# Performance work log

Hardware: AMD Instinct MI355X
Metric: run time of the kernel (lower is better)

The kernel has to match this reference:

```python
import jax, jax.numpy as jnp
import numpy as np

IN_FEATURES = 4096
OUT_FEATURES = 11008


def setup_inputs() -> dict:
    key = jax.random.key(0)
    k1, k2, k3, k4 = jax.random.split(key, 4)
    x = jax.random.normal(k1, (2, 2048, IN_FEATURES), dtype=jnp.float32)
    # two signed int4 values packed per byte: low nibble = even k, high nibble = odd k
    w_packed = jax.random.randint(k2, (OUT_FEATURES, IN_FEATURES // 2), 0, 256, dtype=jnp.int32)
    # rowwise dequant scales (positive, roughly max|w|/7 scale)
    w_scales = jax.random.uniform(k3, (OUT_FEATURES,), dtype=jnp.float32, minval=0.001, maxval=0.02)
    bias = jax.random.normal(k4, (OUT_FEATURES,), dtype=jnp.float32)
    return {"x": x, "w_packed": w_packed, "w_scales": w_scales, "bias": bias}


def _dequantize(w_packed, w_scales):
    # unpack two int4 nibbles per byte
    low = w_packed & 0xF            # [O, K//2]
    high = (w_packed >> 4) & 0xF    # [O, K//2]
    q = jnp.stack([low, high], axis=-1).reshape(w_packed.shape[0], -1)  # [O, K]
    q = jnp.where(q >= 8, q - 16, q)  # sign-extend int4 to [-8, 7]
    return q.astype(w_scales.dtype) * w_scales[:, None]  # [O, K]


def reference(x, w_packed, w_scales, bias):
    w = _dequantize(w_packed, w_scales)               # [O, K] fp32
    y = jnp.einsum('bsk,ok->bso', x, w)               # GEMM
    return y + bias
```

## Files before the change

### kernel.cpp

```cpp
#include <hip/hip_runtime.h>
#include <hip/hip_bf16.h>
#include <stdint.h>

#define M_DIM 4096
#define K_DIM 4096
#define N_DIM 11008
#define KP    2048

#define BK2   64
#define NKT   (K_DIM/BK2)
#define NTM2  (M_DIM/256)
#define NTN2  (N_DIM/256)
#define NBLK2 (NTM2*NTN2)
#define HT_BYTES 8192

#define BM 128
#define BN 128
#define BK 64
#define NTM (M_DIM/BM)
#define NTN (N_DIM/BN)
#define NBLK (NTM*NTN)

typedef __attribute__((ext_vector_type(8)))  short bf16x8;
typedef __attribute__((ext_vector_type(4)))  float f32x4;
typedef __attribute__((ext_vector_type(4)))  int   i32x4;
typedef __attribute__((ext_vector_type(16))) int   i32x16;
typedef __attribute__((ext_vector_type(16))) char  c8x16;
typedef __attribute__((ext_vector_type(8)))  unsigned short u16x8;

typedef const void __attribute__((address_space(1)))* gas_ptr;
typedef void __attribute__((address_space(3)))* las_ptr;

__device__ __forceinline__ void async_copy16(void* lds, const void* g) {
  __builtin_amdgcn_global_load_lds((gas_ptr)g, (las_ptr)lds, 16, 0, 0);
}

__device__ __forceinline__ unsigned short f2bf_rne(float f) {
  uint32_t u = __builtin_bit_cast(uint32_t, f);
  u += 0x7FFFu + ((u >> 16) & 1u);
  return (unsigned short)(u >> 16);
}
__device__ __forceinline__ unsigned short i2bf(int v) {
  float f = (float)v;
  return (unsigned short)(__builtin_bit_cast(uint32_t, f) >> 16);
}
__device__ __forceinline__ int sx4(int b, int which) {
  return ((int)((uint32_t)b << (28 - 4 * which))) >> 28;
}


__global__ __launch_bounds__(256) void rowmax_x(const float* __restrict__ x,
                                                float* __restrict__ xs,
                                                float* __restrict__ xr) {
  const int row = blockIdx.x;
  const int tid = threadIdx.x;
  const float4* r4 = (const float4*)(x + (size_t)row * K_DIM);
  float m = 0.f;
  for (int j = tid; j < K_DIM / 4; j += 256) {
    float4 v = r4[j];
    m = fmaxf(m, fmaxf(fmaxf(fabsf(v.x), fabsf(v.y)), fmaxf(fabsf(v.z), fabsf(v.w))));
  }
  for (int off = 32; off >= 1; off >>= 1) m = fmaxf(m, __shfl_down(m, off));
  __shared__ float sm[4];
  if ((tid & 63) == 0) sm[tid >> 6] = m;
  __syncthreads();
  if (tid == 0) {
    m = fmaxf(fmaxf(sm[0], sm[1]), fmaxf(sm[2], sm[3]));
    xs[row] = m * (1.0f / 127.0f);
    xr[row] = (m > 0.f) ? 127.0f / m : 0.f;
  }
}

__global__ __launch_bounds__(256) void quant_x_tiled(const float* __restrict__ x,
                                                     const float* __restrict__ xr,
                                                     char* __restrict__ wsA) {
  const int total = NTM2 * NKT * 2 * 512;
  for (int i = blockIdx.x * blockDim.x + threadIdx.x; i < total;
       i += gridDim.x * blockDim.x) {
    int rc  = i & 511;
    int h   = (i >> 9) & 1;
    int kt  = (i >> 10) & 63;
    int tm  = i >> 16;
    int row = rc >> 2, e = rc & 3;
    int grow = tm * 256 + h * 128 + row;
    const float4* src = (const float4*)(x + (size_t)grow * K_DIM + kt * 64 + e * 16);
    float4 v0 = src[0], v1 = src[1], v2 = src[2], v3 = src[3];
    float vv[16] = { v0.x, v0.y, v0.z, v0.w, v1.x, v1.y, v1.z, v1.w,
                     v2.x, v2.y, v2.z, v2.w, v3.x, v3.y, v3.z, v3.w };
    const float rs = xr[grow];
    c8x16 q;
#pragma unroll
    for (int j = 0; j < 16; ++j) q[j] = (char)__float2int_rn(vv[j] * rs);
    int c = (row >> 5) * 128 + (e >> 1) * 64 + (e & 1) * 32 + (row & 31);
    *(c8x16*)(wsA + (size_t)(i >> 9) * HT_BYTES + c * 16) = q;
  }
}

__global__ __launch_bounds__(256) void deq_w_i8(const int* __restrict__ wp,
                                                char* __restrict__ wsB) {
  const int total = NTN2 * NKT * 2 * 512;
  for (int i = blockIdx.x * blockDim.x + threadIdx.x; i < total;
       i += gridDim.x * blockDim.x) {
    int rc  = i & 511;
    int h   = (i >> 9) & 1;
    int kt  = (i >> 10) & 63;
    int tn  = i >> 16;
    int row = rc >> 2, e = rc & 3;
    const int4* src = (const int4*)(wp + (size_t)(tn * 256 + h * 128 + row) * KP + kt * 32 + e * 8);
    int4 a = src[0], b = src[1];
    c8x16 q;
    q[0]  = (char)sx4(a.x, 0); q[1]  = (char)sx4(a.x, 1);
    q[2]  = (char)sx4(a.y, 0); q[3]  = (char)sx4(a.y, 1);
    q[4]  = (char)sx4(a.z, 0); q[5]  = (char)sx4(a.z, 1);
    q[6]  = (char)sx4(a.w, 0); q[7]  = (char)sx4(a.w, 1);
    q[8]  = (char)sx4(b.x, 0); q[9]  = (char)sx4(b.x, 1);
    q[10] = (char)sx4(b.y, 0); q[11] = (char)sx4(b.y, 1);
    q[12] = (char)sx4(b.z, 0); q[13] = (char)sx4(b.z, 1);
    q[14] = (char)sx4(b.w, 0); q[15] = (char)sx4(b.w, 1);
    int c = (row >> 5) * 128 + (e >> 1) * 64 + (e & 1) * 32 + (row & 31);
    *(c8x16*)(wsB + (size_t)(i >> 9) * HT_BYTES + c * 16) = q;
  }
}

__global__ __launch_bounds__(512, 2)
void qgemm8i(const char* __restrict__ wsA, const char* __restrict__ wsB,
             const float* __restrict__ xs,
             const float* __restrict__ scales, const float* __restrict__ bias,
             float* __restrict__ out) {
  __shared__ __align__(16) char smem[65536];

  const int tid  = threadIdx.x;
  const int lane = tid & 63, wid = tid >> 6;
  const int wr = wid >> 2, wc = wid & 3;
  const int l31 = lane & 31, kg = lane >> 5;

  int bid = blockIdx.x;
  int id  = (bid & 7) * (NBLK2 / 8) + (bid >> 3);
  int tm  = id & (NTM2 - 1), tn = id >> 4;

  const char* gA = wsA + (size_t)tm * (NKT * 2) * HT_BYTES;
  const char* gB = wsB + (size_t)tn * (NKT * 2) * HT_BYTES;

  const char* baseA = smem + wr * HT_BYTES + lane * 16;
  const char* baseB = smem + 16384 + (wc >> 1) * HT_BYTES + lane * 16;

#define STAGE(ldsoff, src) \
    async_copy16(smem + (ldsoff) + wid * 1024, (src) + wid * 1024 + lane * 16)
#define STAGE_A(buf, h, kt) STAGE((buf) * 32768 + (h) * HT_BYTES, gA + ((kt) * 2 + (h)) * HT_BYTES)
#define STAGE_B(buf, h, kt) STAGE((buf) * 32768 + 16384 + (h) * HT_BYTES, gB + ((kt) * 2 + (h)) * HT_BYTES)

  i32x16 acc[4][2] = {};
  i32x4  aS0[2][2], aS1[2][2];
  i32x4  bS0[2], bS1[2];

#define LDA_SET(dst, buf, sel) do { \
    _Pragma("unroll") for (int i = 0; i < 2; ++i) \
    _Pragma("unroll") for (int ks = 0; ks < 2; ++ks) \
      dst[i][ks] = *(const i32x4*)(baseA + (buf) * 32768 + ((sel) * 2 + i) * 2048 + ks * 1024); \
  } while (0)
#define LDB_SET(dst, buf, bn) do { \
    _Pragma("unroll") for (int ks = 0; ks < 2; ++ks) \
      dst[ks] = *(const i32x4*)(baseB + (buf) * 32768 + ((wc & 1) * 2 + (bn)) * 2048 + ks * 1024); \
  } while (0)
#define MMQ(aS, bS, sel, bn) do { \
    _Pragma("unroll") for (int ks = 0; ks < 2; ++ks) \
    _Pragma("unroll") for (int i = 0; i < 2; ++i) \
      acc[(sel) * 2 + i][bn] = __builtin_amdgcn_mfma_i32_32x32x32_i8( \
          aS[i][ks], bS[ks], acc[(sel) * 2 + i][bn], 0, 0, 0); \
  } while (0)

#define PH_BAR __builtin_amdgcn_s_barrier()
#define LGKM0 asm volatile("s_waitcnt lgkmcnt(0)" ::: "memory")
#define VMC1  asm volatile("s_waitcnt vmcnt(1)" ::: "memory")
#define VMC2  asm volatile("s_waitcnt vmcnt(2)" ::: "memory")
#define PRIO1 __builtin_amdgcn_s_setprio(1)
#define PRIO0 __builtin_amdgcn_s_setprio(0)

  STAGE_B(0, 0, 0); STAGE_B(0, 1, 0);
  STAGE_A(0, 0, 0); STAGE_A(0, 1, 0);
  STAGE_B(1, 0, 1); STAGE_B(1, 1, 1);
  VMC2;
  PH_BAR;
  LDA_SET(aS0, 0, 0); LDB_SET(bS0, 0, 0);

  for (int t = 0; t < NKT / 2; ++t) {
    const int k1 = 2 * t + 1;
    const int k2 = (2 * t + 2 < NKT) ? 2 * t + 2 : NKT - 1;
    const int k3 = (2 * t + 3 < NKT) ? 2 * t + 3 : NKT - 1;

    LGKM0; PRIO1; MMQ(aS0, bS0, 0, 0); PRIO0;
    STAGE_A(1, 0, k1);
    LDB_SET(bS1, 0, 1);
    PH_BAR;
    LGKM0; PRIO1; MMQ(aS0, bS1, 0, 1); PRIO0;
    STAGE_A(1, 1, k1);
    LDA_SET(aS1, 0, 1);
    PH_BAR;
    LGKM0; PRIO1; MMQ(aS1, bS1, 1, 1); PRIO0;
    STAGE_B(0, 0, k2);
    VMC1;
    PH_BAR;
    PRIO1; MMQ(aS1, bS0, 1, 0); PRIO0;
    STAGE_B(0, 1, k2);
    LDA_SET(aS0, 1, 0); LDB_SET(bS0, 1, 0);
    PH_BAR;
    LGKM0; PRIO1; MMQ(aS0, bS0, 0, 0); PRIO0;
    STAGE_A(0, 0, k2);
    LDB_SET(bS1, 1, 1);
    PH_BAR;
    LGKM0; PRIO1; MMQ(aS0, bS1, 0, 1); PRIO0;
    STAGE_A(0, 1, k2);
    LDA_SET(aS1, 1, 1);
    PH_BAR;
    LGKM0; PRIO1; MMQ(aS1, bS1, 1, 1); PRIO0;
    STAGE_B(1, 0, k3);
    VMC1;
    PH_BAR;
    PRIO1; MMQ(aS1, bS0, 1, 0); PRIO0;
    STAGE_B(1, 1, k3);
    LDA_SET(aS0, 0, 0); LDB_SET(bS0, 0, 0);
    PH_BAR;
  }

  const int m0 = tm * 256, n0 = tn * 256;
#pragma unroll
  for (int ni = 0; ni < 2; ++ni) {
    const int o = n0 + wc * 64 + ni * 32 + l31;
    const float sw = scales[o];
    const float b = bias[o];
#pragma unroll
    for (int mi = 0; mi < 4; ++mi) {
      const int mrb = m0 + wr * 128 + mi * 32 + kg * 4;
#pragma unroll
      for (int r = 0; r < 16; ++r) {
        const int mr = mrb + (r & 3) + 8 * (r >> 2);
        const float y = (float)acc[mi][ni][r] * xs[mr] * sw + b;
        __builtin_nontemporal_store(y, out + (size_t)mr * N_DIM + o);
      }
    }
  }
#undef STAGE
#undef STAGE_A
#undef STAGE_B
#undef LDA_SET
#undef LDB_SET
#undef MMQ
#undef PH_BAR
#undef LGKM0
#undef VMC1
#undef VMC2
#undef PRIO1
#undef PRIO0
}

__global__ __launch_bounds__(256) void cvt_x_kernel(const float* __restrict__ x,
                                                    unsigned short* __restrict__ xb) {
  const int n4 = M_DIM * K_DIM / 4;
  int i = blockIdx.x * blockDim.x + threadIdx.x;
  const int stride = gridDim.x * blockDim.x;
  for (; i < n4; i += stride) {
    float4 v = ((const float4*)x)[i];
    ushort4 r;
    r.x = f2bf_rne(v.x); r.y = f2bf_rne(v.y);
    r.z = f2bf_rne(v.z); r.w = f2bf_rne(v.w);
    ((ushort4*)xb)[i] = r;
  }
}

template <int MODE>
__global__ __launch_bounds__(256)
void qgemm_kernel(const float* __restrict__ x, const unsigned short* __restrict__ xb,
                  const int* __restrict__ wp,
                  const float* __restrict__ scales, const float* __restrict__ bias,
                  float* __restrict__ out) {
  __shared__ __align__(16) unsigned short As[BM * BK];
  __shared__ __align__(16) unsigned short Bs[BN * BK];
  const int tid  = threadIdx.x;
  const int lane = tid & 63;
  const int wid  = tid >> 6;
  int bid = blockIdx.x;
  int swzb = (bid & 7) * (NBLK / 8) + (bid >> 3);
  const int tm = swzb & (NTM - 1);
  const int tn = swzb >> 5;
  const int m0 = tm * BM, n0 = tn * BN;
  const int wr = wid >> 1, wc = wid & 1;
  const int fr = lane & 15;
  const int fg = lane >> 4;
  f32x4 acc[4][4] = {};

  for (int kt = 0; kt < K_DIM / BK; ++kt) {
    int4   breg[4];
    float4 areg[8];
#pragma unroll
    for (int p = 0; p < 4; ++p) {
      int fl = p * 256 + tid;
      int row = fl >> 3, u = fl & 7;
      breg[p] = *(const int4*)(wp + (size_t)(n0 + row) * KP + kt * (BK / 2) + u * 4);
    }
    if constexpr (MODE == 2) {
#pragma unroll
      for (int p = 0; p < 8; ++p) {
        int fl = p * 256 + tid;
        int row = fl >> 4, u = fl & 15;
        areg[p] = *(const float4*)(x + (size_t)(m0 + row) * K_DIM + kt * BK + u * 4);
      }
    }
    __syncthreads();
    if constexpr (MODE == 1) {
#pragma unroll
      for (int p = 0; p < 4; ++p) {
        int t16 = p * 256 + tid;
        int row = t16 >> 3, u = t16 & 7;
        const unsigned short* g = xb + (size_t)(m0 + row) * K_DIM + kt * BK + u * 8;
        async_copy16((char*)As + (p * 256 + wid * 64) * 16, g);
      }
    } else {
#pragma unroll
      for (int p = 0; p < 8; ++p) {
        int fl = p * 256 + tid;
        int row = fl >> 4, u = fl & 15;
        ushort4 r;
        r.x = f2bf_rne(areg[p].x); r.y = f2bf_rne(areg[p].y);
        r.z = f2bf_rne(areg[p].z); r.w = f2bf_rne(areg[p].w);
        *(ushort4*)((char*)As + row * 128 + u * 8) = r;
      }
    }
#pragma unroll
    for (int p = 0; p < 4; ++p) {
      int fl = p * 256 + tid;
      int row = fl >> 3, u = fl & 7;
      int4 b = breg[p];
      u16x8 r;
      r[0] = i2bf(sx4(b.x, 0)); r[1] = i2bf(sx4(b.x, 1));
      r[2] = i2bf(sx4(b.y, 0)); r[3] = i2bf(sx4(b.y, 1));
      r[4] = i2bf(sx4(b.z, 0)); r[5] = i2bf(sx4(b.z, 1));
      r[6] = i2bf(sx4(b.w, 0)); r[7] = i2bf(sx4(b.w, 1));
      *(u16x8*)((char*)Bs + row * 128 + u * 16) = r;
    }
    __syncthreads();
#pragma unroll
    for (int kk = 0; kk < 2; ++kk) {
      const int kb = kk * 64 + fg * 16;
      bf16x8 af[4], bfv[4];
#pragma unroll
      for (int mi = 0; mi < 4; ++mi) {
        int row = wr * 64 + mi * 16 + fr;
        af[mi] = *(const bf16x8*)((const char*)As + row * 128 + kb);
      }
#pragma unroll
      for (int ni = 0; ni < 4; ++ni) {
        int row = wc * 64 + ni * 16 + fr;
        bfv[ni] = *(const bf16x8*)((const char*)Bs + row * 128 + kb);
      }
#pragma unroll
      for (int mi = 0; mi < 4; ++mi)
#pragma unroll
        for (int ni = 0; ni < 4; ++ni)
          acc[mi][ni] = __builtin_amdgcn_mfma_f32_16x16x32_bf16(af[mi], bfv[ni], acc[mi][ni], 0, 0, 0);
    }
  }
#pragma unroll
  for (int ni = 0; ni < 4; ++ni) {
    const int o = n0 + wc * 64 + ni * 16 + fr;
    const float s = scales[o];
    const float b = bias[o];
#pragma unroll
    for (int mi = 0; mi < 4; ++mi) {
      const int mr = m0 + wr * 64 + mi * 16 + fg * 4;
#pragma unroll
      for (int r = 0; r < 4; ++r)
        out[(size_t)(mr + r) * N_DIM + o] = acc[mi][ni][r] * s + b;
    }
  }
}

extern "C" void kernel_launch(void* const* d_in, const int* in_sizes, int n_in,
                              void* d_out, int out_size, void* d_ws, size_t ws_size,
                              hipStream_t stream) {
  const float* x  = (const float*)d_in[0];
  const int*   wp = (const int*)d_in[1];
  const float* sc = (const float*)d_in[2];
  const float* bs = (const float*)d_in[3];
  float* out = (float*)d_out;

  const size_t a_bytes  = (size_t)NTM2 * NKT * 2 * HT_BYTES;
  const size_t b_bytes  = (size_t)NTN2 * NKT * 2 * HT_BYTES;
  const size_t xs_bytes = (size_t)M_DIM * 4;
  char*  wsA = (char*)d_ws;
  char*  wsB = (char*)d_ws + a_bytes;
  float* xs  = (float*)((char*)d_ws + a_bytes + b_bytes);
  float* xr  = xs + M_DIM;

  if (ws_size >= a_bytes + b_bytes + 2 * xs_bytes) {
    rowmax_x<<<M_DIM, 256, 0, stream>>>(x, xs, xr);
    quant_x_tiled<<<2048, 256, 0, stream>>>(x, xr, wsA);
    deq_w_i8<<<2048, 256, 0, stream>>>(wp, wsB);
    qgemm8i<<<NBLK2, 512, 0, stream>>>(wsA, wsB, xs, sc, bs, out);
  } else if (ws_size >= (size_t)M_DIM * K_DIM * 2) {
    cvt_x_kernel<<<2048, 256, 0, stream>>>(x, (unsigned short*)d_ws);
    qgemm_kernel<1><<<NBLK, 256, 0, stream>>>(x, (unsigned short*)d_ws, wp, sc, bs, out);
  } else {
    qgemm_kernel<2><<<NBLK, 256, 0, stream>>>(x, (unsigned short*)d_ws, wp, sc, bs, out);
  }
}
```

Before: 265.2 us.

## Fuse x rowmax with int8 quantization and coarsen GEMM main-loop phases

Combines the activation row-max kernel and the tiled int8 quantization kernel into one per-row kernel, so x is read once and one launch and the xr buffer go away. Separately, the int8 MFMA main loop is restructured from eight barrier phases per two K-tiles to four, issuing two MFMA groups and both stage copies per phase and preloading both B fragments. This cuts barrier count at the cost of holding more fragments in registers and a coarser overlap between copies and compute. The wait on outstanding global-to-LDS loads also changes from vmcnt(1) to vmcnt(2).

```diff
diff --git a/kernel.cpp b/kernel.cpp
--- a/kernel.cpp
+++ b/kernel.cpp
@@ -49,51 +49,33 @@
 }
 
 
-__global__ __launch_bounds__(256) void rowmax_x(const float* __restrict__ x,
-                                                float* __restrict__ xs,
-                                                float* __restrict__ xr) {
-  const int row = blockIdx.x;
-  const int tid = threadIdx.x;
-  const float4* r4 = (const float4*)(x + (size_t)row * K_DIM);
+__global__ __launch_bounds__(256) void quant_x_fused(const float* __restrict__ x,
+                                                     char* __restrict__ wsA,
+                                                     float* __restrict__ xs) {
+  const int grow = blockIdx.x;
+  const int tid  = threadIdx.x;
+  const float4* src = (const float4*)(x + (size_t)grow * K_DIM + tid * 16);
+  float4 v0 = src[0], v1 = src[1], v2 = src[2], v3 = src[3];
+  float vv[16] = { v0.x, v0.y, v0.z, v0.w, v1.x, v1.y, v1.z, v1.w,
+                   v2.x, v2.y, v2.z, v2.w, v3.x, v3.y, v3.z, v3.w };
   float m = 0.f;
-  for (int j = tid; j < K_DIM / 4; j += 256) {
-    float4 v = r4[j];
-    m = fmaxf(m, fmaxf(fmaxf(fabsf(v.x), fabsf(v.y)), fmaxf(fabsf(v.z), fabsf(v.w))));
-  }
-  for (int off = 32; off >= 1; off >>= 1) m = fmaxf(m, __shfl_down(m, off));
+#pragma unroll
+  for (int j = 0; j < 16; ++j) m = fmaxf(m, fabsf(vv[j]));
+#pragma unroll
+  for (int off = 32; off >= 1; off >>= 1) m = fmaxf(m, __shfl_xor(m, off));
   __shared__ float sm[4];
   if ((tid & 63) == 0) sm[tid >> 6] = m;
   __syncthreads();
-  if (tid == 0) {
-    m = fmaxf(fmaxf(sm[0], sm[1]), fmaxf(sm[2], sm[3]));
-    xs[row] = m * (1.0f / 127.0f);
-    xr[row] = (m > 0.f) ? 127.0f / m : 0.f;
-  }
-}
-
-__global__ __launch_bounds__(256) void quant_x_tiled(const float* __restrict__ x,
-                                                     const float* __restrict__ xr,
-                                                     char* __restrict__ wsA) {
-  const int total = NTM2 * NKT * 2 * 512;
-  for (int i = blockIdx.x * blockDim.x + threadIdx.x; i < total;
-       i += gridDim.x * blockDim.x) {
-    int rc  = i & 511;
-    int h   = (i >> 9) & 1;
-    int kt  = (i >> 10) & 63;
-    int tm  = i >> 16;
-    int row = rc >> 2, e = rc & 3;
-    int grow = tm * 256 + h * 128 + row;
-    const float4* src = (const float4*)(x + (size_t)grow * K_DIM + kt * 64 + e * 16);
-    float4 v0 = src[0], v1 = src[1], v2 = src[2], v3 = src[3];
-    float vv[16] = { v0.x, v0.y, v0.z, v0.w, v1.x, v1.y, v1.z, v1.w,
-                     v2.x, v2.y, v2.z, v2.w, v3.x, v3.y, v3.z, v3.w };
-    const float rs = xr[grow];
-    c8x16 q;
-#pragma unroll
-    for (int j = 0; j < 16; ++j) q[j] = (char)__float2int_rn(vv[j] * rs);
-    int c = (row >> 5) * 128 + (e >> 1) * 64 + (e & 1) * 32 + (row & 31);
-    *(c8x16*)(wsA + (size_t)(i >> 9) * HT_BYTES + c * 16) = q;
-  }
+  m = fmaxf(fmaxf(sm[0], sm[1]), fmaxf(sm[2], sm[3]));
+  const float rs = (m > 0.f) ? 127.0f / m : 0.f;
+  if (tid == 0) xs[grow] = m * (1.0f / 127.0f);
+  c8x16 q;
+#pragma unroll
+  for (int j = 0; j < 16; ++j) q[j] = (char)__float2int_rn(vv[j] * rs);
+  const int kt = tid >> 2, e = tid & 3;
+  const int tm = grow >> 8, wi = grow & 255, h = wi >> 7, r = wi & 127;
+  const int c = (r >> 5) * 128 + (e >> 1) * 64 + (e & 1) * 32 + (r & 31);
+  *(c8x16*)(wsA + ((size_t)(tm * NKT + kt) * 2 + h) * HT_BYTES + c * 16) = q;
 }
 
 __global__ __launch_bounds__(256) void deq_w_i8(const int* __restrict__ wp,
@@ -171,7 +153,6 @@
 
 #define PH_BAR __builtin_amdgcn_s_barrier()
 #define LGKM0 asm volatile("s_waitcnt lgkmcnt(0)" ::: "memory")
-#define VMC1  asm volatile("s_waitcnt vmcnt(1)" ::: "memory")
 #define VMC2  asm volatile("s_waitcnt vmcnt(2)" ::: "memory")
 #define PRIO1 __builtin_amdgcn_s_setprio(1)
 #define PRIO0 __builtin_amdgcn_s_setprio(0)
@@ -181,44 +162,34 @@
   STAGE_B(1, 0, 1); STAGE_B(1, 1, 1);
   VMC2;
   PH_BAR;
-  LDA_SET(aS0, 0, 0); LDB_SET(bS0, 0, 0);
+  LDA_SET(aS0, 0, 0); LDB_SET(bS0, 0, 0); LDB_SET(bS1, 0, 1);
 
   for (int t = 0; t < NKT / 2; ++t) {
     const int k1 = 2 * t + 1;
     const int k2 = (2 * t + 2 < NKT) ? 2 * t + 2 : NKT - 1;
     const int k3 = (2 * t + 3 < NKT) ? 2 * t + 3 : NKT - 1;
 
-    LGKM0; PRIO1; MMQ(aS0, bS0, 0, 0); PRIO0;
-    STAGE_A(1, 0, k1);
-    LDB_SET(bS1, 0, 1);
-    PH_BAR;
-    LGKM0; PRIO1; MMQ(aS0, bS1, 0, 1); PRIO0;
-    STAGE_A(1, 1, k1);
+    LGKM0;
+    PRIO1; MMQ(aS0, bS0, 0, 0); MMQ(aS0, bS1, 0, 1); PRIO0;
+    STAGE_A(1, 0, k1); STAGE_A(1, 1, k1);
     LDA_SET(aS1, 0, 1);
     PH_BAR;
-    LGKM0; PRIO1; MMQ(aS1, bS1, 1, 1); PRIO0;
-    STAGE_B(0, 0, k2);
-    VMC1;
+    LGKM0;
+    PRIO1; MMQ(aS1, bS1, 1, 1); MMQ(aS1, bS0, 1, 0); PRIO0;
+    STAGE_B(0, 0, k2); STAGE_B(0, 1, k2);
+    VMC2;
+    LDA_SET(aS0, 1, 0); LDB_SET(bS0, 1, 0); LDB_SET(bS1, 1, 1);
     PH_BAR;
-    PRIO1; MMQ(aS1, bS0, 1, 0); PRIO0;
-    STAGE_B(0, 1, k2);
-    LDA_SET(aS0, 1, 0); LDB_SET(bS0, 1, 0);
-    PH_BAR;
-    LGKM0; PRIO1; MMQ(aS0, bS0, 0, 0); PRIO0;
-    STAGE_A(0, 0, k2);
-    LDB_SET(bS1, 1, 1);
-    PH_BAR;
-    LGKM0; PRIO1; MMQ(aS0, bS1, 0, 1); PRIO0;
-    STAGE_A(0, 1, k2);
+    LGKM0;
+    PRIO1; MMQ(aS0, bS0, 0, 0); MMQ(aS0, bS1, 0, 1); PRIO0;
+    STAGE_A(0, 0, k2); STAGE_A(0, 1, k2);
     LDA_SET(aS1, 1, 1);
     PH_BAR;
-    LGKM0; PRIO1; MMQ(aS1, bS1, 1, 1); PRIO0;
-    STAGE_B(1, 0, k3);
-    VMC1;
-    PH_BAR;
-    PRIO1; MMQ(aS1, bS0, 1, 0); PRIO0;
-    STAGE_B(1, 1, k3);
-    LDA_SET(aS0, 0, 0); LDB_SET(bS0, 0, 0);
+    LGKM0;
+    PRIO1; MMQ(aS1, bS1, 1, 1); MMQ(aS1, bS0, 1, 0); PRIO0;
+    STAGE_B(1, 0, k3); STAGE_B(1, 1, k3);
+    VMC2;
+    LDA_SET(aS0, 0, 0); LDB_SET(bS0, 0, 0); LDB_SET(bS1, 0, 1);
     PH_BAR;
   }
 
@@ -247,7 +218,6 @@
 #undef MMQ
 #undef PH_BAR
 #undef LGKM0
-#undef VMC1
 #undef VMC2
 #undef PRIO1
 #undef PRIO0
@@ -389,11 +359,9 @@
   char*  wsA = (char*)d_ws;
   char*  wsB = (char*)d_ws + a_bytes;
   float* xs  = (float*)((char*)d_ws + a_bytes + b_bytes);
-  float* xr  = xs + M_DIM;
-
-  if (ws_size >= a_bytes + b_bytes + 2 * xs_bytes) {
-    rowmax_x<<<M_DIM, 256, 0, stream>>>(x, xs, xr);
-    quant_x_tiled<<<2048, 256, 0, stream>>>(x, xr, wsA);
+
+  if (ws_size >= a_bytes + b_bytes + xs_bytes) {
+    quant_x_fused<<<M_DIM, 256, 0, stream>>>(x, wsA, xs);
     deq_w_i8<<<2048, 256, 0, stream>>>(wp, wsB);
     qgemm8i<<<NBLK2, 512, 0, stream>>>(wsA, wsB, xs, sc, bs, out);
   } else if (ws_size >= (size_t)M_DIM * K_DIM * 2) {
```

Result: faster. 247.3 us (median of 3 runs) (-6.8%).
